# Performance work log

Measured on AMD Instinct MI355X. Metric: run time of the kernel, lower is better.

Reference implementation:

```python
import jax, jax.numpy as jnp
import numpy as np

B, C_IN, C_OUT, H, F_DIM = 32, 64, 1, 4096, 8
OUT_CH, K = F_DIM + 1, F_DIM // 2 + 1          # even-feature branch: 9 channels, kernel (1,5)
HALF = F_DIM * (F_DIM + 1) // 2                # 36 upper-triangular entries
MIN_VEC = 0.001
IU = np.triu_indices(F_DIM)                    # torch.triu_indices(f, f)


def setup_inputs() -> dict:
    key = jax.random.key(0)
    k1, k2, k3, k4, k5 = jax.random.split(key, 5)
    x = jax.random.normal(k1, (B, C_IN, H, F_DIM), jnp.float32)
    w_n = jax.random.normal(k2, (C_OUT, C_IN, 1, 1), jnp.float32) * 0.05
    b_n = jax.random.normal(k3, (C_OUT,), jnp.float32) * 0.05
    w_p = jax.random.normal(k4, (OUT_CH, C_IN, 1, K), jnp.float32) * 0.05
    b_p = jax.random.normal(k5, (OUT_CH,), jnp.float32) * 0.05
    return {"x": x, "w_n": w_n, "b_n": b_n, "w_p": w_p, "b_p": b_p}


def _forward(x, w_n, b_n, w_p, b_p):
    # n_conv: 1x1 conv -> softplus  (loc: [B, C_OUT, H, F_DIM])
    loc = jax.nn.softplus(
        jnp.einsum('bchw,oc->bohw', x, w_n[:, :, 0, 0]) + b_n[None, :, None, None])
    # p_conv: (1,K) valid conv -> softplus  (scale: [B, OUT_CH, H, W_out])
    p = jax.lax.conv_general_dilated(
        x, w_p, window_strides=(1, 1), padding='VALID',
        dimension_numbers=('NCHW', 'OIHW', 'NCHW')) + b_p[None, :, None, None]
    scale = jax.nn.softplus(p)
    # unsqueeze(1) + permute(0,1,3,2,4) + flatten(start_dim=3) -> [B,1,H,HALF]
    sigma = jnp.transpose(scale, (0, 2, 1, 3)).reshape(B, 1, H, HALF)
    # scatter upper-tri values symmetrically into [B,1,H,F,F]
    z = jnp.zeros((B, 1, H, F_DIM, F_DIM), sigma.dtype)
    z = z.at[..., IU[0], IU[1]].set(sigma)
    z = z.at[..., IU[1], IU[0]].set(sigma)
    # batched eigh, clamp eigenvalues, reconstruct PD matrix, symmetrize
    eigval, eigvec = jnp.linalg.eigh(z)
    clamped = jnp.maximum(eigval, MIN_VEC)
    pd = jnp.einsum('...ij,...j,...kj->...ik', eigvec, clamped, eigvec)
    pd = 0.5 * (pd + jnp.swapaxes(pd, -1, -2))
    return loc, pd


def reference(x, w_n, b_n, w_p, b_p):
    return _forward(x, w_n, b_n, w_p, b_p)
```

## Files before the change

### kernel.cpp

```cpp
#include <hip/hip_runtime.h>
#include <math.h>

#define B_      32
#define C_IN    64
#define H_      4096
#define F_      8
#define OUT_CH  9
#define KW      5
#define BH      (B_ * H_)
#define LOC_N   (BH * F_)
#define NSWEEP  6
#define MIN_VEC 0.001f

__device__ const int PAIRS[7][4][2] = {
  {{0,7},{1,6},{2,5},{3,4}},
  {{0,6},{5,7},{1,4},{2,3}},
  {{0,5},{4,6},{3,7},{1,2}},
  {{0,4},{3,5},{2,6},{1,7}},
  {{0,3},{2,4},{1,5},{6,7}},
  {{0,2},{1,3},{4,7},{5,6}},
  {{0,1},{2,7},{3,6},{4,5}},
};

#define SYM(i,j) (((i) < (j)) ? A[i][j] : A[j][i])

__device__ __forceinline__ float softplus_f(float v) {
    return fmaxf(v, 0.0f) + __logf(1.0f + __expf(-fabsf(v)));
}

__global__ __launch_bounds__(256, 2)
void mgauss_fused(const float* __restrict__ x,
                  const float* __restrict__ w_n,
                  const float* __restrict__ b_n,
                  const float* __restrict__ w_p,
                  const float* __restrict__ b_p,
                  float* __restrict__ out)
{
    const int t = blockIdx.x * 256 + threadIdx.x;
    const int b = t >> 12;
    const int h = t & 4095;

    const float* xp = x + ((size_t)b * C_IN * H_ + h) * F_;

    float la[F_];
    #pragma unroll
    for (int w = 0; w < F_; ++w) la[w] = 0.0f;
    float pa[OUT_CH][4];
    #pragma unroll
    for (int o = 0; o < OUT_CH; ++o)
        #pragma unroll
        for (int wo = 0; wo < 4; ++wo) pa[o][wo] = 0.0f;

    #pragma unroll 4
    for (int c = 0; c < C_IN; ++c) {
        const float4 x0 = *(const float4*)(xp + (size_t)c * (H_ * F_));
        const float4 x1 = *(const float4*)(xp + (size_t)c * (H_ * F_) + 4);
        const float xa[F_] = {x0.x, x0.y, x0.z, x0.w, x1.x, x1.y, x1.z, x1.w};

        const float wn = w_n[c];
        #pragma unroll
        for (int w = 0; w < F_; ++w) la[w] = fmaf(xa[w], wn, la[w]);

        #pragma unroll
        for (int o = 0; o < OUT_CH; ++o) {
            #pragma unroll
            for (int k = 0; k < KW; ++k) {
                const float wv = w_p[(o * C_IN + c) * KW + k];
                #pragma unroll
                for (int wo = 0; wo < 4; ++wo)
                    pa[o][wo] = fmaf(xa[wo + k], wv, pa[o][wo]);
            }
        }
    }

    {
        const float bn = b_n[0];
        float lv[F_];
        #pragma unroll
        for (int w = 0; w < F_; ++w) lv[w] = softplus_f(la[w] + bn);
        float* lo = out + (size_t)t * F_;
        *(float4*)(lo)     = make_float4(lv[0], lv[1], lv[2], lv[3]);
        *(float4*)(lo + 4) = make_float4(lv[4], lv[5], lv[6], lv[7]);
    }

    float A[F_][F_];
    {
        float sig[36];
        #pragma unroll
        for (int o = 0; o < OUT_CH; ++o) {
            const float bp = b_p[o];
            #pragma unroll
            for (int wo = 0; wo < 4; ++wo)
                sig[o * 4 + wo] = softplus_f(pa[o][wo] + bp);
        }
        int k = 0;
        #pragma unroll
        for (int i = 0; i < F_; ++i)
            #pragma unroll
            for (int j = i; j < F_; ++j) {
                A[i][j] = sig[k];
                ++k;
            }
    }

    float V[F_][F_];
    #pragma unroll
    for (int i = 0; i < F_; ++i)
        #pragma unroll
        for (int j = 0; j < F_; ++j)
            V[i][j] = (i == j) ? 1.0f : 0.0f;

    for (int sweep = 0; sweep < NSWEEP; ++sweep) {
        #pragma unroll
        for (int r = 0; r < 7; ++r) {
            float cs[4], sn[4], tv[4];
            #pragma unroll
            for (int j = 0; j < 4; ++j) {
                const int p = PAIRS[r][j][0], q = PAIRS[r][j][1];
                const float apq = A[p][q];
                const float app = A[p][p];
                const float aqq = A[q][q];
                float th = (aqq - app) / (2.0f * apq);
                float tt = 1.0f / (fabsf(th) + sqrtf(fmaf(th, th, 1.0f)));
                tt = (th < 0.0f) ? -tt : tt;
                tt = (apq == 0.0f) ? 0.0f : tt;
                const float cc = 1.0f / sqrtf(fmaf(tt, tt, 1.0f));
                cs[j] = cc; sn[j] = tt * cc; tv[j] = tt;
            }
            #pragma unroll
            for (int j = 0; j < 4; ++j) {
                const int p = PAIRS[r][j][0], q = PAIRS[r][j][1];
                const float cc = cs[j], ss = sn[j], tt = tv[j];
                const float apq = A[p][q];
                A[p][p] = fmaf(-tt, apq, A[p][p]);
                A[q][q] = fmaf( tt, apq, A[q][q]);
                A[p][q] = 0.0f;
                #pragma unroll
                for (int i = 0; i < F_; ++i) {
                    if (i == p || i == q) continue;
                    const float aip = SYM(i, p);
                    const float aiq = SYM(i, q);
                    SYM(i, p) = fmaf(-ss, aiq, cc * aip);
                    SYM(i, q) = fmaf( ss, aip, cc * aiq);
                }
            }
            #pragma unroll
            for (int j = 0; j < 4; ++j) {
                const int p = PAIRS[r][j][0], q = PAIRS[r][j][1];
                const float cc = cs[j], ss = sn[j];
                #pragma unroll
                for (int i = 0; i < F_; ++i) {
                    const float u = V[i][p], v = V[i][q];
                    V[i][p] = fmaf(-ss, v, cc * u);
                    V[i][q] = fmaf( ss, u, cc * v);
                }
            }
        }
    }

    float lam[F_];
    #pragma unroll
    for (int k = 0; k < F_; ++k) lam[k] = fmaxf(A[k][k], MIN_VEC);

    float W[F_][F_];
    #pragma unroll
    for (int i = 0; i < F_; ++i)
        #pragma unroll
        for (int k = 0; k < F_; ++k)
            W[i][k] = V[i][k] * lam[k];

    float PD[F_][F_];
    #pragma unroll
    for (int i = 0; i < F_; ++i) {
        #pragma unroll
        for (int j = i; j < F_; ++j) {
            float acc = 0.0f;
            #pragma unroll
            for (int k = 0; k < F_; ++k)
                acc = fmaf(W[i][k], V[j][k], acc);
            PD[i][j] = acc;
            PD[j][i] = acc;
        }
    }

    float* po = out + LOC_N + (size_t)t * (F_ * F_);
    #pragma unroll
    for (int i = 0; i < F_; ++i) {
        *(float4*)(po + i * F_)     = make_float4(PD[i][0], PD[i][1], PD[i][2], PD[i][3]);
        *(float4*)(po + i * F_ + 4) = make_float4(PD[i][4], PD[i][5], PD[i][6], PD[i][7]);
    }
}

extern "C" void kernel_launch(void* const* d_in, const int* in_sizes, int n_in,
                              void* d_out, int out_size, void* d_ws, size_t ws_size,
                              hipStream_t stream) {
    const float* x   = (const float*)d_in[0];
    const float* w_n = (const float*)d_in[1];
    const float* b_n = (const float*)d_in[2];
    const float* w_p = (const float*)d_in[3];
    const float* b_p = (const float*)d_in[4];
    float* out = (float*)d_out;

    dim3 grid(BH / 256);
    dim3 block(256);
    hipLaunchKernelGGL(mgauss_fused, grid, block, 0, stream,
                       x, w_n, b_n, w_p, b_p, out);
}
```

Measured before the change: 458.0 us.

## Split fused kernel into channel-parallel conv stage and separate eigen stage

Splits the fused kernel in two. The first kernel spreads the 64 input channels across 8 lanes per output row and combines the partial sums with wavefront xor-shuffles; it writes loc directly and the softplus sigma values to a workspace buffer. The second kernel reads sigma and runs the Jacobi eigen-decomposition and the PD reconstruction. This gives the memory-bound convolution more parallelism and a smaller register footprint, which allows higher occupancy. The cost is an extra round trip of about 19 MB through global memory and a second launch, and the old fused kernel remains as a fallback when the workspace is too small.

```diff
diff --git a/kernel.cpp b/kernel.cpp
--- a/kernel.cpp
+++ b/kernel.cpp
@@ -11,6 +11,7 @@
 #define LOC_N   (BH * F_)
 #define NSWEEP  6
 #define MIN_VEC 0.001f
+#define SIG_STRIDE 36
 
 __device__ const int PAIRS[7][4][2] = {
   {{0,7},{1,6},{2,5},{3,4}},
@@ -26,6 +27,204 @@
 
 __device__ __forceinline__ float softplus_f(float v) {
     return fmaxf(v, 0.0f) + __logf(1.0f + __expf(-fabsf(v)));
+}
+
+__global__ __launch_bounds__(256, 5)
+void conv_stage(const float* __restrict__ x,
+                const float* __restrict__ w_n,
+                const float* __restrict__ b_n,
+                const float* __restrict__ w_p,
+                const float* __restrict__ b_p,
+                float* __restrict__ loc_out,
+                float* __restrict__ sig)
+{
+    const int lane = threadIdx.x & 63;
+    const int wv   = threadIdx.x >> 6;
+    const int p    = lane & 7;
+    const int cg   = lane >> 3;
+    const int t    = blockIdx.x * 32 + wv * 8 + p;
+    const int b    = t >> 12;
+    const int h    = t & 4095;
+
+    const float* xp = x + (((size_t)b * C_IN + (size_t)cg * 8) * H_ + h) * F_;
+
+    float la[F_];
+    #pragma unroll
+    for (int w = 0; w < F_; ++w) la[w] = 0.0f;
+    float pa[OUT_CH][4];
+    #pragma unroll
+    for (int o = 0; o < OUT_CH; ++o)
+        #pragma unroll
+        for (int wo = 0; wo < 4; ++wo) pa[o][wo] = 0.0f;
+
+    #pragma unroll
+    for (int cc = 0; cc < 8; ++cc) {
+        const float4 x0 = *(const float4*)(xp + (size_t)cc * (H_ * F_));
+        const float4 x1 = *(const float4*)(xp + (size_t)cc * (H_ * F_) + 4);
+        const float xa[F_] = {x0.x, x0.y, x0.z, x0.w, x1.x, x1.y, x1.z, x1.w};
+        const int c = cg * 8 + cc;
+
+        const float wn = w_n[c];
+        #pragma unroll
+        for (int w = 0; w < F_; ++w) la[w] = fmaf(xa[w], wn, la[w]);
+
+        const float* wpp = w_p + c * KW;
+        #pragma unroll
+        for (int o = 0; o < OUT_CH; ++o) {
+            #pragma unroll
+            for (int k = 0; k < KW; ++k) {
+                const float wval = wpp[o * (C_IN * KW) + k];
+                #pragma unroll
+                for (int wo = 0; wo < 4; ++wo)
+                    pa[o][wo] = fmaf(xa[wo + k], wval, pa[o][wo]);
+            }
+        }
+    }
+
+    #pragma unroll
+    for (int m = 8; m <= 32; m <<= 1) {
+        #pragma unroll
+        for (int w = 0; w < F_; ++w) la[w] += __shfl_xor(la[w], m, 64);
+        #pragma unroll
+        for (int o = 0; o < OUT_CH; ++o)
+            #pragma unroll
+            for (int wo = 0; wo < 4; ++wo)
+                pa[o][wo] += __shfl_xor(pa[o][wo], m, 64);
+    }
+
+    if (cg == 0) {
+        const float bn = b_n[0];
+        float lv[F_];
+        #pragma unroll
+        for (int w = 0; w < F_; ++w) lv[w] = softplus_f(la[w] + bn);
+        float* lo = loc_out + (size_t)t * F_;
+        *(float4*)(lo)     = make_float4(lv[0], lv[1], lv[2], lv[3]);
+        *(float4*)(lo + 4) = make_float4(lv[4], lv[5], lv[6], lv[7]);
+
+        float* sp = sig + (size_t)t * SIG_STRIDE;
+        #pragma unroll
+        for (int o = 0; o < OUT_CH; ++o) {
+            const float bp = b_p[o];
+            float4 s = make_float4(softplus_f(pa[o][0] + bp),
+                                   softplus_f(pa[o][1] + bp),
+                                   softplus_f(pa[o][2] + bp),
+                                   softplus_f(pa[o][3] + bp));
+            *(float4*)(sp + o * 4) = s;
+        }
+    }
+}
+
+__global__ __launch_bounds__(256, 2)
+void eig_stage(const float* __restrict__ sig, float* __restrict__ out)
+{
+    const int t = blockIdx.x * 256 + threadIdx.x;
+
+    float sf[36];
+    {
+        const float* sp = sig + (size_t)t * SIG_STRIDE;
+        #pragma unroll
+        for (int j = 0; j < 9; ++j) {
+            const float4 v = *(const float4*)(sp + j * 4);
+            sf[j * 4 + 0] = v.x; sf[j * 4 + 1] = v.y;
+            sf[j * 4 + 2] = v.z; sf[j * 4 + 3] = v.w;
+        }
+    }
+
+    float A[F_][F_];
+    {
+        int k = 0;
+        #pragma unroll
+        for (int i = 0; i < F_; ++i)
+            #pragma unroll
+            for (int j = i; j < F_; ++j) { A[i][j] = sf[k]; ++k; }
+    }
+
+    float V[F_][F_];
+    #pragma unroll
+    for (int i = 0; i < F_; ++i)
+        #pragma unroll
+        for (int j = 0; j < F_; ++j)
+            V[i][j] = (i == j) ? 1.0f : 0.0f;
+
+    for (int sweep = 0; sweep < NSWEEP; ++sweep) {
+        #pragma unroll
+        for (int r = 0; r < 7; ++r) {
+            float cs[4], sn[4], tv[4];
+            #pragma unroll
+            for (int j = 0; j < 4; ++j) {
+                const int p = PAIRS[r][j][0], q = PAIRS[r][j][1];
+                const float apq = A[p][q];
+                const float app = A[p][p];
+                const float aqq = A[q][q];
+                float th = (aqq - app) / (2.0f * apq);
+                float tt = 1.0f / (fabsf(th) + sqrtf(fmaf(th, th, 1.0f)));
+                tt = (th < 0.0f) ? -tt : tt;
+                tt = (apq == 0.0f) ? 0.0f : tt;
+                const float cc = 1.0f / sqrtf(fmaf(tt, tt, 1.0f));
+                cs[j] = cc; sn[j] = tt * cc; tv[j] = tt;
+            }
+            #pragma unroll
+            for (int j = 0; j < 4; ++j) {
+                const int p = PAIRS[r][j][0], q = PAIRS[r][j][1];
+                const float cc = cs[j], ss = sn[j], tt = tv[j];
+                const float apq = A[p][q];
+                A[p][p] = fmaf(-tt, apq, A[p][p]);
+                A[q][q] = fmaf( tt, apq, A[q][q]);
+                A[p][q] = 0.0f;
+                #pragma unroll
+                for (int i = 0; i < F_; ++i) {
+                    if (i == p || i == q) continue;
+                    const float aip = SYM(i, p);
+                    const float aiq = SYM(i, q);
+                    SYM(i, p) = fmaf(-ss, aiq, cc * aip);
+                    SYM(i, q) = fmaf( ss, aip, cc * aiq);
+                }
+            }
+            #pragma unroll
+            for (int j = 0; j < 4; ++j) {
+                const int p = PAIRS[r][j][0], q = PAIRS[r][j][1];
+                const float cc = cs[j], ss = sn[j];
+                #pragma unroll
+                for (int i = 0; i < F_; ++i) {
+                    const float u = V[i][p], v = V[i][q];
+                    V[i][p] = fmaf(-ss, v, cc * u);
+                    V[i][q] = fmaf( ss, u, cc * v);
+                }
+            }
+        }
+    }
+
+    float lam[F_];
+    #pragma unroll
+    for (int k = 0; k < F_; ++k) lam[k] = fmaxf(A[k][k], MIN_VEC);
+
+    float W[F_][F_];
+    #pragma unroll
+    for (int i = 0; i < F_; ++i)
+        #pragma unroll
+        for (int k = 0; k < F_; ++k)
+            W[i][k] = V[i][k] * lam[k];
+
+    float PD[F_][F_];
+    #pragma unroll
+    for (int i = 0; i < F_; ++i) {
+        #pragma unroll
+        for (int j = i; j < F_; ++j) {
+            float acc = 0.0f;
+            #pragma unroll
+            for (int k = 0; k < F_; ++k)
+                acc = fmaf(W[i][k], V[j][k], acc);
+            PD[i][j] = acc;
+            PD[j][i] = acc;
+        }
+    }
+
+    float* po = out + LOC_N + (size_t)t * (F_ * F_);
+    #pragma unroll
+    for (int i = 0; i < F_; ++i) {
+        *(float4*)(po + i * F_)     = make_float4(PD[i][0], PD[i][1], PD[i][2], PD[i][3]);
+        *(float4*)(po + i * F_ + 4) = make_float4(PD[i][4], PD[i][5], PD[i][6], PD[i][7]);
+    }
 }
 
 __global__ __launch_bounds__(256, 2)
@@ -39,7 +238,6 @@
     const int t = blockIdx.x * 256 + threadIdx.x;
     const int b = t >> 12;
     const int h = t & 4095;
-
     const float* xp = x + ((size_t)b * C_IN * H_ + h) * F_;
 
     float la[F_];
@@ -56,21 +254,18 @@
         const float4 x0 = *(const float4*)(xp + (size_t)c * (H_ * F_));
         const float4 x1 = *(const float4*)(xp + (size_t)c * (H_ * F_) + 4);
         const float xa[F_] = {x0.x, x0.y, x0.z, x0.w, x1.x, x1.y, x1.z, x1.w};
-
         const float wn = w_n[c];
         #pragma unroll
         for (int w = 0; w < F_; ++w) la[w] = fmaf(xa[w], wn, la[w]);
-
-        #pragma unroll
-        for (int o = 0; o < OUT_CH; ++o) {
+        #pragma unroll
+        for (int o = 0; o < OUT_CH; ++o)
             #pragma unroll
             for (int k = 0; k < KW; ++k) {
-                const float wv = w_p[(o * C_IN + c) * KW + k];
+                const float wval = w_p[(o * C_IN + c) * KW + k];
                 #pragma unroll
                 for (int wo = 0; wo < 4; ++wo)
-                    pa[o][wo] = fmaf(xa[wo + k], wv, pa[o][wo]);
-            }
-        }
+                    pa[o][wo] = fmaf(xa[wo + k], wval, pa[o][wo]);
+            }
     }
 
     {
@@ -85,22 +280,19 @@
 
     float A[F_][F_];
     {
-        float sig[36];
+        float sigv[36];
         #pragma unroll
         for (int o = 0; o < OUT_CH; ++o) {
             const float bp = b_p[o];
             #pragma unroll
             for (int wo = 0; wo < 4; ++wo)
-                sig[o * 4 + wo] = softplus_f(pa[o][wo] + bp);
+                sigv[o * 4 + wo] = softplus_f(pa[o][wo] + bp);
         }
         int k = 0;
         #pragma unroll
         for (int i = 0; i < F_; ++i)
             #pragma unroll
-            for (int j = i; j < F_; ++j) {
-                A[i][j] = sig[k];
-                ++k;
-            }
+            for (int j = i; j < F_; ++j) { A[i][j] = sigv[k]; ++k; }
     }
 
     float V[F_][F_];
@@ -118,9 +310,7 @@
             for (int j = 0; j < 4; ++j) {
                 const int p = PAIRS[r][j][0], q = PAIRS[r][j][1];
                 const float apq = A[p][q];
-                const float app = A[p][p];
-                const float aqq = A[q][q];
-                float th = (aqq - app) / (2.0f * apq);
+                float th = (A[q][q] - A[p][p]) / (2.0f * apq);
                 float tt = 1.0f / (fabsf(th) + sqrtf(fmaf(th, th, 1.0f)));
                 tt = (th < 0.0f) ? -tt : tt;
                 tt = (apq == 0.0f) ? 0.0f : tt;
@@ -161,14 +351,12 @@
     float lam[F_];
     #pragma unroll
     for (int k = 0; k < F_; ++k) lam[k] = fmaxf(A[k][k], MIN_VEC);
-
     float W[F_][F_];
     #pragma unroll
     for (int i = 0; i < F_; ++i)
         #pragma unroll
         for (int k = 0; k < F_; ++k)
             W[i][k] = V[i][k] * lam[k];
-
     float PD[F_][F_];
     #pragma unroll
     for (int i = 0; i < F_; ++i) {
@@ -182,7 +370,6 @@
             PD[j][i] = acc;
         }
     }
-
     float* po = out + LOC_N + (size_t)t * (F_ * F_);
     #pragma unroll
     for (int i = 0; i < F_; ++i) {
@@ -201,8 +388,15 @@
     const float* b_p = (const float*)d_in[4];
     float* out = (float*)d_out;
 
-    dim3 grid(BH / 256);
-    dim3 block(256);
-    hipLaunchKernelGGL(mgauss_fused, grid, block, 0, stream,
-                       x, w_n, b_n, w_p, b_p, out);
+    const size_t need = (size_t)BH * SIG_STRIDE * sizeof(float);
+    if (ws_size >= need) {
+        float* sig = (float*)d_ws;
+        hipLaunchKernelGGL(conv_stage, dim3(BH / 32), dim3(256), 0, stream,
+                           x, w_n, b_n, w_p, b_p, out, sig);
+        hipLaunchKernelGGL(eig_stage, dim3(BH / 256), dim3(256), 0, stream,
+                           sig, out);
+    } else {
+        hipLaunchKernelGGL(mgauss_fused, dim3(BH / 256), dim3(256), 0, stream,
+                           x, w_n, b_n, w_p, b_p, out);
+    }
 }
```

New measurement: 493.8 us. 1.08x slower.

## Split channel reduction across four waves with shared-memory partial sums

Applied to the files above, without the earlier changes.

Each block now handles 64 output positions, and its four wavefronts each reduce 16 of the 64 input channels. Partial conv sums go through shared memory and wave 0 adds them up, then runs the Jacobi eigen-solve and writes the outputs. This gives four times as many blocks and spreads the bandwidth-heavy conv stage over more waves. The trade-off is that only a quarter of the threads run the serial eigh stage, while three waves sit idle after the barrier. It also adds shared memory per block and raises the launch-bounds occupancy hint.

```diff
diff --git a/kernel.cpp b/kernel.cpp
--- a/kernel.cpp
+++ b/kernel.cpp
@@ -28,19 +28,24 @@
     return fmaxf(v, 0.0f) + __logf(1.0f + __expf(-fabsf(v)));
 }
 
-__global__ __launch_bounds__(256, 2)
-void mgauss_fused(const float* __restrict__ x,
+__global__ __launch_bounds__(256, 3)
+void mgauss_block(const float* __restrict__ x,
                   const float* __restrict__ w_n,
                   const float* __restrict__ b_n,
                   const float* __restrict__ w_p,
                   const float* __restrict__ b_p,
                   float* __restrict__ out)
 {
-    const int t = blockIdx.x * 256 + threadIdx.x;
-    const int b = t >> 12;
-    const int h = t & 4095;
-
-    const float* xp = x + ((size_t)b * C_IN * H_ + h) * F_;
+    __shared__ float part[3][64][48];
+
+    const int lane = threadIdx.x & 63;
+    const int wv   = threadIdx.x >> 6;
+    const int t    = blockIdx.x * 64 + lane;
+    const int b    = t >> 12;
+    const int h    = t & 4095;
+    const int c0   = wv * 16;
+
+    const float* xp = x + (((size_t)b * C_IN + c0) * H_ + h) * F_;
 
     float la[F_];
     #pragma unroll
@@ -52,10 +57,11 @@
         for (int wo = 0; wo < 4; ++wo) pa[o][wo] = 0.0f;
 
     #pragma unroll 4
-    for (int c = 0; c < C_IN; ++c) {
-        const float4 x0 = *(const float4*)(xp + (size_t)c * (H_ * F_));
-        const float4 x1 = *(const float4*)(xp + (size_t)c * (H_ * F_) + 4);
+    for (int cc = 0; cc < 16; ++cc) {
+        const float4 x0 = *(const float4*)(xp + (size_t)cc * (H_ * F_));
+        const float4 x1 = *(const float4*)(xp + (size_t)cc * (H_ * F_) + 4);
         const float xa[F_] = {x0.x, x0.y, x0.z, x0.w, x1.x, x1.y, x1.z, x1.w};
+        const int c = c0 + cc;
 
         const float wn = w_n[c];
         #pragma unroll
@@ -65,11 +71,37 @@
         for (int o = 0; o < OUT_CH; ++o) {
             #pragma unroll
             for (int k = 0; k < KW; ++k) {
-                const float wv = w_p[(o * C_IN + c) * KW + k];
+                const float wval = w_p[(o * C_IN + c) * KW + k];
                 #pragma unroll
                 for (int wo = 0; wo < 4; ++wo)
-                    pa[o][wo] = fmaf(xa[wo + k], wv, pa[o][wo]);
-            }
+                    pa[o][wo] = fmaf(xa[wo + k], wval, pa[o][wo]);
+            }
+        }
+    }
+
+    if (wv > 0) {
+        float* dst = &part[wv - 1][lane][0];
+        ((float4*)dst)[0] = make_float4(la[0], la[1], la[2], la[3]);
+        ((float4*)dst)[1] = make_float4(la[4], la[5], la[6], la[7]);
+        #pragma unroll
+        for (int o = 0; o < OUT_CH; ++o)
+            ((float4*)dst)[2 + o] = make_float4(pa[o][0], pa[o][1],
+                                                pa[o][2], pa[o][3]);
+    }
+    __syncthreads();
+    if (wv != 0) return;
+
+    #pragma unroll
+    for (int w = 0; w < 3; ++w) {
+        const float* src = &part[w][lane][0];
+        const float4 a0 = ((const float4*)src)[0];
+        const float4 a1 = ((const float4*)src)[1];
+        la[0] += a0.x; la[1] += a0.y; la[2] += a0.z; la[3] += a0.w;
+        la[4] += a1.x; la[5] += a1.y; la[6] += a1.z; la[7] += a1.w;
+        #pragma unroll
+        for (int o = 0; o < OUT_CH; ++o) {
+            const float4 v = ((const float4*)src)[2 + o];
+            pa[o][0] += v.x; pa[o][1] += v.y; pa[o][2] += v.z; pa[o][3] += v.w;
         }
     }
 
@@ -97,10 +129,7 @@
         #pragma unroll
         for (int i = 0; i < F_; ++i)
             #pragma unroll
-            for (int j = i; j < F_; ++j) {
-                A[i][j] = sig[k];
-                ++k;
-            }
+            for (int j = i; j < F_; ++j) { A[i][j] = sig[k]; ++k; }
     }
 
     float V[F_][F_];
@@ -201,8 +230,6 @@
     const float* b_p = (const float*)d_in[4];
     float* out = (float*)d_out;
 
-    dim3 grid(BH / 256);
-    dim3 block(256);
-    hipLaunchKernelGGL(mgauss_fused, grid, block, 0, stream,
+    hipLaunchKernelGGL(mgauss_block, dim3(BH / 64), dim3(256), 0, stream,
                        x, w_n, b_n, w_p, b_p, out);
 }
```

New measurement: 533.0 us. 1.16x slower.
